# Performance work log

Measured on AMD Instinct MI355X. Metric: run time of the kernel, lower is better.

Reference implementation:

```python
import jax, jax.numpy as jnp
import numpy as np
from jax import lax

EPS = 1e-5
TEM = 10.0  # self.tem at init; tem_proportion buffer is 0 so it stays 10.0


def _conv1d(x, w, padding, dilation=1, groups=1):
    # x: [B, C, S], w: [O, I//groups, K]
    return lax.conv_general_dilated(
        x, w, window_strides=(1,), padding=[(padding, padding)],
        rhs_dilation=(dilation,), dimension_numbers=('NCH', 'OIH', 'NCH'),
        feature_group_count=groups)


def _bn(y, gamma, beta):
    # training-mode BatchNorm1d: stats over (batch, length) per channel
    m = y.mean(axis=(0, 2), keepdims=True)
    v = y.var(axis=(0, 2), keepdims=True)
    return (y - m) * lax.rsqrt(v + EPS) * gamma[None, :, None] + beta[None, :, None]


def _nor_conv(x, w, g, b, k):
    return _bn(_conv1d(jax.nn.relu(x), w, padding=k // 2), g, b)


def _dil_conv(x, wd, wp, g, b, k):
    C = x.shape[1]
    y = _conv1d(jax.nn.relu(x), wd, padding=k - 1, dilation=2, groups=C)
    y = _conv1d(y, wp, padding=0)
    return _bn(y, g, b)


def _avg_pool3(x):
    s = lax.reduce_window(x, 0.0, lax.add, (1, 1, 3), (1, 1, 1),
                          [(0, 0), (0, 0), (1, 1)])
    return s / 3.0  # count_include_pad=True


def _max_pool3(x):
    return lax.reduce_window(x, -jnp.inf, lax.max, (1, 1, 3), (1, 1, 1),
                             [(0, 0), (0, 0), (1, 1)])


def _forward(x, u, arch_parameters,
             w_nor3, g_nor3, b_nor3, w_nor5, g_nor5, b_nor5,
             w_nor7, g_nor7, b_nor7,
             wd_dil3, wp_dil3, g_dil3, b_dil3,
             wd_dil5, wp_dil5, g_dil5, b_dil5,
             wd_dil7, wp_dil7, g_dil7, b_dil7):
    # ---- Gumbel straight-through gate (get_gumbel_prob) ----
    uc = jnp.clip(u, 1e-9, 1.0 - 1e-9)
    gumbels = -jnp.log(-jnp.log(uc))  # -log(Exp(1) sample)
    logits = (jax.nn.log_softmax(arch_parameters, axis=1) + gumbels) / TEM
    probs = jax.nn.softmax(logits, axis=1)          # [1, 10]
    index = jnp.argmax(probs, axis=-1)              # [1]
    one_h = jax.nn.one_hot(index, probs.shape[-1], dtype=probs.dtype)
    hardwts = one_h - lax.stop_gradient(probs) + probs  # straight-through

    # ---- forward_gdas: single edge (max_nodes=2) ----
    xc = jnp.transpose(x, (0, 2, 1))  # [B, H, S]: hidden=channels, seq=length
    branches = [
        lambda t: jnp.zeros_like(t),                         # none
        _avg_pool3,                                          # avg_pool_3
        _max_pool3,                                          # max_pool_3
        lambda t: _nor_conv(t, w_nor3, g_nor3, b_nor3, 3),   # nor_conv_3
        lambda t: _nor_conv(t, w_nor5, g_nor5, b_nor5, 5),   # nor_conv_5
        lambda t: _nor_conv(t, w_nor7, g_nor7, b_nor7, 7),   # nor_conv_7
        lambda t: _dil_conv(t, wd_dil3, wp_dil3, g_dil3, b_dil3, 3),
        lambda t: _dil_conv(t, wd_dil5, wp_dil5, g_dil5, b_dil5, 5),
        lambda t: _dil_conv(t, wd_dil7, wp_dil7, g_dil7, b_dil7, 7),
        lambda t: t,                                         # skip_connect
    ]
    idx = index[0]
    w = hardwts[0]                                  # [10]
    sel = lax.switch(idx, branches, xc)             # only argmax op is run
    w_sel = jnp.take(w, idx)
    # GDAS: w[argmax]*op(x) + sum of remaining scalar weights (broadcast add)
    out = w_sel * sel + (jnp.sum(w) - w_sel)
    out = jnp.transpose(out, (0, 2, 1))             # back to [B, S, H]
    return out + x                                  # residual


def setup_inputs() -> dict:
    key = jax.random.key(0)
    ks = jax.random.split(key, 16)
    B, S, H = 8, 512, 768
    d = {
        'x': jax.random.normal(ks[0], (B, S, H), jnp.float32),
        'u': jax.random.uniform(ks[1], (1, 10), jnp.float32),
        'arch_parameters': 0.001 * jax.random.normal(ks[2], (1, 10), jnp.float32),
    }
    i = 3
    for k in (3, 5, 7):
        d[f'w_nor{k}'] = 0.02 * jax.random.normal(ks[i], (H, H, k), jnp.float32); i += 1
        d[f'g_nor{k}'] = jnp.ones((H,), jnp.float32)
        d[f'b_nor{k}'] = jnp.zeros((H,), jnp.float32)
    for k in (3, 5, 7):
        d[f'wd_dil{k}'] = 0.1 * jax.random.normal(ks[i], (H, 1, k), jnp.float32); i += 1
        d[f'wp_dil{k}'] = 0.02 * jax.random.normal(ks[i], (H, H, 1), jnp.float32); i += 1
        d[f'g_dil{k}'] = jnp.ones((H,), jnp.float32)
        d[f'b_dil{k}'] = jnp.zeros((H,), jnp.float32)
    return d


def reference(x, u, arch_parameters,
              w_nor3, g_nor3, b_nor3, w_nor5, g_nor5, b_nor5,
              w_nor7, g_nor7, b_nor7,
              wd_dil3, wp_dil3, g_dil3, b_dil3,
              wd_dil5, wp_dil5, g_dil5, b_dil5,
              wd_dil7, wp_dil7, g_dil7, b_dil7):
    return _forward(x, u, arch_parameters,
                    w_nor3, g_nor3, b_nor3, w_nor5, g_nor5, b_nor5,
                    w_nor7, g_nor7, b_nor7,
                    wd_dil3, wp_dil3, g_dil3, b_dil3,
                    wd_dil5, wp_dil5, g_dil5, b_dil5,
                    wd_dil7, wp_dil7, g_dil7, b_dil7)
```

## Files before the change

### kernel.cpp

```cpp
#include <hip/hip_runtime.h>
#include <math.h>

#define BB 8
#define SS 512
#define HH 768
#define NTOT (BB*SS*HH)
#define EPSBN 1e-5f
#define SPAD 4
#define SROWS (SS + 2*SPAD)

typedef __attribute__((ext_vector_type(8))) short short8v;
typedef __attribute__((ext_vector_type(4))) float float4v;

struct Params {
  const float *x, *u, *ap;
  const float *w_nor3, *g_nor3, *b_nor3;
  const float *w_nor5, *g_nor5, *b_nor5;
  const float *w_nor7, *g_nor7, *b_nor7;
  const float *wd3, *wp3, *gd3, *bd3;
  const float *wd5, *wp5, *gd5, *bd5;
  const float *wd7, *wp7, *gd7, *bd7;
  float *out;
  float *hdr;
  float *y;
  short *xb;
  short *wb;
  float *psum;
  float *psq;
};

__device__ __forceinline__ short f2bf(float f) {
  union { float f; unsigned u; } v; v.f = f;
  unsigned r = v.u + 0x7FFF + ((v.u >> 16) & 1);
  return (short)(r >> 16);
}

__device__ __forceinline__ void gate_compute(const float* __restrict__ apg,
                                             const float* __restrict__ ug,
                                             int& idx_out, float& wsel_out) {
  float ap[10], lg[10], pr[10];
  float mx = -INFINITY;
  for (int i = 0; i < 10; i++) { ap[i] = apg[i]; mx = fmaxf(mx, ap[i]); }
  float se = 0.f;
  for (int i = 0; i < 10; i++) se += expf(ap[i] - mx);
  float lse = mx + logf(se);
  float lmax = -INFINITY;
  for (int i = 0; i < 10; i++) {
    float uc = fminf(fmaxf(ug[i], 1e-9f), 1.f - 1e-9f);
    float gb = -logf(-logf(uc));
    lg[i] = ((ap[i] - lse) + gb) * 0.1f;
    lmax = fmaxf(lmax, lg[i]);
  }
  float ps = 0.f;
  for (int i = 0; i < 10; i++) { pr[i] = expf(lg[i] - lmax); ps += pr[i]; }
  int idx = 0; float best = -INFINITY;
  for (int i = 0; i < 10; i++) {
    pr[i] /= ps;
    if (pr[i] > best) { best = pr[i]; idx = i; }
  }
  idx_out = idx;
  wsel_out = (1.0f - pr[idx]) + pr[idx];
}

#define NITEMS_A (BB * SROWS * 96)
#define NITEMS   (NITEMS_A + HH * 96)
#define PREP_BLOCKS 512

template<int K>
__device__ __forceinline__ void wprep(const float* __restrict__ W, short* __restrict__ wb,
                                      int o, int i0) {
  const float* src = W + ((size_t)o * HH + i0) * K;
  float f[8 * K];
#pragma unroll
  for (int j = 0; j < 2 * K; j++) ((float4*)f)[j] = ((const float4*)src)[j];
#pragma unroll
  for (int dk = 0; dk < K; dk++) {
    short8v o8;
#pragma unroll
    for (int j = 0; j < 8; j++) o8[j] = f2bf(f[j * K + dk]);
    *(short8v*)(wb + ((size_t)dk * HH + o) * HH + i0) = o8;
  }
}

__global__ __launch_bounds__(256) void prep_kernel(Params p) {
  __shared__ int sh_idx;
  int t = threadIdx.x;
  if (t == 0) {
    int idx; float wsel;
    gate_compute(p.ap, p.u, idx, wsel);
    sh_idx = idx;
    if (blockIdx.x == 0) {
      p.hdr[0] = wsel;
      p.hdr[1] = 0.0f;
      ((int*)p.hdr)[2] = idx;
    }
  }
  __syncthreads();
  int idx = sh_idx;
  if (idx < 3 || idx > 8) return;

  if (blockIdx.x == 0) {
    for (int i = t; i < HH; i += 256) { p.psum[i] = 0.f; p.psq[i] = 0.f; }
  }

  for (int u = blockIdx.x * 256 + t; u < NITEMS; u += PREP_BLOCKS * 256) {
    if (u < NITEMS_A) {
      int c0 = (u % 96) * 8;
      int row = (u / 96) % SROWS;
      int b = u / (96 * SROWS);
      int s = row - SPAD;
      short8v o8 = (short8v){0,0,0,0,0,0,0,0};
      if (s >= 0 && s < SS) {
        float v[8];
        if (idx <= 5) {
          const float* xp = p.x + ((size_t)(b * SS + s) * HH + c0);
          float4 f0 = ((const float4*)xp)[0];
          float4 f1 = ((const float4*)xp)[1];
          v[0] = fmaxf(f0.x, 0.f); v[1] = fmaxf(f0.y, 0.f);
          v[2] = fmaxf(f0.z, 0.f); v[3] = fmaxf(f0.w, 0.f);
          v[4] = fmaxf(f1.x, 0.f); v[5] = fmaxf(f1.y, 0.f);
          v[6] = fmaxf(f1.z, 0.f); v[7] = fmaxf(f1.w, 0.f);
        } else {
          int k = 3 + 2 * (idx - 6);
          const float* wd = (idx == 6) ? p.wd3 : (idx == 7) ? p.wd5 : p.wd7;
#pragma unroll
          for (int j = 0; j < 8; j++) v[j] = 0.f;
          for (int dk = 0; dk < k; dk++) {
            int ss = s + 2 * dk - (k - 1);
            if (ss < 0 || ss >= SS) continue;
            const float* xp = p.x + ((size_t)(b * SS + ss) * HH + c0);
            float4 f0 = ((const float4*)xp)[0];
            float4 f1 = ((const float4*)xp)[1];
            float ff[8] = {f0.x, f0.y, f0.z, f0.w, f1.x, f1.y, f1.z, f1.w};
#pragma unroll
            for (int j = 0; j < 8; j++)
              v[j] += fmaxf(ff[j], 0.f) * wd[(c0 + j) * k + dk];
          }
        }
#pragma unroll
        for (int j = 0; j < 8; j++) o8[j] = f2bf(v[j]);
      }
      *(short8v*)(p.xb + (size_t)(b * SROWS + row) * HH + c0) = o8;
    } else {
      int u2 = u - NITEMS_A;
      int i0 = (u2 % 96) * 8;
      int o = u2 / 96;
      if (idx == 3)      wprep<3>(p.w_nor3, p.wb, o, i0);
      else if (idx == 4) wprep<5>(p.w_nor5, p.wb, o, i0);
      else if (idx == 5) wprep<7>(p.w_nor7, p.wb, o, i0);
      else wprep<1>((idx == 6) ? p.wp3 : (idx == 7) ? p.wp5 : p.wp7, p.wb, o, i0);
    }
  }
}

#define BM 128
#define BN 64
#define BK 64
#define AROWS 136

typedef const __attribute__((address_space(1))) unsigned int* gas_t;
typedef __attribute__((address_space(3))) unsigned int* las_t;
__device__ __forceinline__ void gload16(const void* g, void* l) {
  __builtin_amdgcn_global_load_lds((gas_t)g, (las_t)l, 16, 0, 0);
}

__global__ __launch_bounds__(256, 3) void conv_gemm_kernel(Params p) {
  int idx = ((const int*)p.hdr)[2];
  if (idx < 3 || idx > 8) return;
  bool nor = (idx <= 5);
  int taps = nor ? (3 + 2 * (idx - 3)) : 1;
  int halo = nor ? (taps >> 1) : 0;

  __shared__ __attribute__((aligned(16))) short As[AROWS * BK];
  __shared__ __attribute__((aligned(16))) short Bs[4 * BN * BK];

  int mt = blockIdx.x;
  int b = mt >> 2;
  int s0 = (mt & 3) * BM;
  int o0 = blockIdx.y * BN;

  int t = threadIdx.x;
  int lane = t & 63;
  int w = t >> 6;
  int l16 = lane & 15, quad = lane >> 4;
  int wm0 = (w >> 1) * 64;
  int wn0 = (w & 1) * 32;
  int lr = lane >> 3;
  int sw8 = ((lane & 7) ^ lr) * 8;

  const short* Ag[4];
  int abrow = b * SROWS + s0 + 8 * w + lr;
#pragma unroll
  for (int j = 0; j < 4; j++)
    Ag[j] = p.xb + (size_t)(abrow + 32 * j) * HH + sw8;
  const short* Agp = p.xb + (size_t)(b * SROWS + s0 + 128 + lr) * HH + sw8;
  const short* Bg = p.wb + (size_t)(o0 + 8 * w + lr) * HH + sw8;

  short* Asl[4];
#pragma unroll
  for (int j = 0; j < 4; j++) Asl[j] = &As[(32 * j + 8 * w) * BK];
  short* Aslp = &As[128 * BK];

  float4v acc[4][2];
#pragma unroll
  for (int mi = 0; mi < 4; mi++)
#pragma unroll
    for (int ni = 0; ni < 2; ni++) acc[mi][ni] = (float4v){0.f, 0.f, 0.f, 0.f};

  const char* Ac = (const char*)As;
  const char* Bc = (const char*)Bs;
  int bb[2][2];
#pragma unroll
  for (int ni = 0; ni < 2; ni++)
#pragma unroll
    for (int h = 0; h < 2; h++)
      bb[ni][h] = (wn0 + ni * 16 + l16) * (2 * BK) + (((h * 4 + quad) ^ (l16 & 7)) << 4);

  int np0 = taps < 4 ? taps : 4;
  int np1 = taps - np0;

  auto mm = [&](int dk, int pl) {
    int doff = dk - halo + 4;
    int rowA = wm0 + l16 + doff;
    int xr = (l16 + doff) & 7;
    int a0 = rowA * 128 + ((quad ^ xr) << 4);
    int a1 = rowA * 128 + (((4 + quad) ^ xr) << 4);
    short8v af0[4], af1[4], bf0[2], bf1[2];
#pragma unroll
    for (int mi = 0; mi < 4; mi++) {
      af0[mi] = *(const short8v*)(Ac + a0 + mi * 2048);
      af1[mi] = *(const short8v*)(Ac + a1 + mi * 2048);
    }
    int pb = pl * 8192;
#pragma unroll
    for (int ni = 0; ni < 2; ni++) {
      bf0[ni] = *(const short8v*)(Bc + pb + bb[ni][0]);
      bf1[ni] = *(const short8v*)(Bc + pb + bb[ni][1]);
    }
#pragma unroll
    for (int mi = 0; mi < 4; mi++)
#pragma unroll
      for (int ni = 0; ni < 2; ni++)
        acc[mi][ni] = __builtin_amdgcn_mfma_f32_16x16x32_bf16(af0[mi], bf0[ni], acc[mi][ni], 0, 0, 0);
#pragma unroll
    for (int mi = 0; mi < 4; mi++)
#pragma unroll
      for (int ni = 0; ni < 2; ni++)
        acc[mi][ni] = __builtin_amdgcn_mfma_f32_16x16x32_bf16(af1[mi], bf1[ni], acc[mi][ni], 0, 0, 0);
  };

  for (int k0 = 0; k0 < HH; k0 += BK) {
#pragma unroll
    for (int j = 0; j < 4; j++) gload16(Ag[j] + k0, Asl[j]);
    if (w == 0) gload16(Agp + k0, Aslp);
    for (int pl = 0; pl < np0; pl++) {
      const short* src = Bg + (size_t)pl * HH * HH + k0;
      gload16(src, &Bs[pl * 4096 + w * 512]);
      gload16(src + (size_t)32 * HH, &Bs[pl * 4096 + 2048 + w * 512]);
    }
    __syncthreads();
    for (int dk = 0; dk < np0; dk++) mm(dk, dk);
    __syncthreads();
    if (np1 > 0) {
      for (int pl = 0; pl < np1; pl++) {
        const short* src = Bg + (size_t)(4 + pl) * HH * HH + k0;
        gload16(src, &Bs[pl * 4096 + w * 512]);
        gload16(src + (size_t)32 * HH, &Bs[pl * 4096 + 2048 + w * 512]);
      }
      __syncthreads();
      for (int dk = 0; dk < np1; dk++) mm(4 + dk, dk);
      __syncthreads();
    }
  }

#pragma unroll
  for (int mi = 0; mi < 4; mi++)
#pragma unroll
    for (int ni = 0; ni < 2; ni++) {
      int col = o0 + wn0 + ni * 16 + l16;
#pragma unroll
      for (int r = 0; r < 4; r++) {
        int row = s0 + wm0 + mi * 16 + quad * 4 + r;
        p.y[((size_t)(b * SS + row)) * HH + col] = acc[mi][ni][r];
      }
    }

#pragma unroll
  for (int ni = 0; ni < 2; ni++) {
    float s = 0.f, q = 0.f;
#pragma unroll
    for (int mi = 0; mi < 4; mi++)
#pragma unroll
      for (int r = 0; r < 4; r++) { float v = acc[mi][ni][r]; s += v; q += v * v; }
    s += __shfl_xor(s, 16); s += __shfl_xor(s, 32);
    q += __shfl_xor(q, 16); q += __shfl_xor(q, 32);
    if (lane < 16) {
      int col = o0 + wn0 + ni * 16 + l16;
      atomicAdd(&p.psum[col], s);
      atomicAdd(&p.psq[col], q);
    }
  }
}

#define EPI_BLOCKS 1536
__global__ __launch_bounds__(256) void epilogue_kernel(Params p) {
  int idx = ((const int*)p.hdr)[2];
  float w_sel = p.hdr[0], w_rest = p.hdr[1];
  for (int t4 = blockIdx.x * 256 + threadIdx.x; t4 < NTOT / 4; t4 += EPI_BLOCKS * 256) {
    int base = t4 * 4;
    float4 xv = *(const float4*)(p.x + base);
    float4 sel;
    if (idx >= 3 && idx <= 8) {
      const float* g = (idx == 3) ? p.g_nor3 : (idx == 4) ? p.g_nor5 : (idx == 5) ? p.g_nor7
                     : (idx == 6) ? p.gd3 : (idx == 7) ? p.gd5 : p.gd7;
      const float* be = (idx == 3) ? p.b_nor3 : (idx == 4) ? p.b_nor5 : (idx == 5) ? p.b_nor7
                      : (idx == 6) ? p.bd3 : (idx == 7) ? p.bd5 : p.bd7;
      int c = base % HH;
      float4 yv = *(const float4*)(p.y + base);
      float4 ps = *(const float4*)(p.psum + c);
      float4 pq = *(const float4*)(p.psq + c);
      float4 gv = *(const float4*)(g + c);
      float4 bv = *(const float4*)(be + c);
      const float inv = 1.f / 4096.f;
      float m0 = ps.x * inv, m1 = ps.y * inv, m2 = ps.z * inv, m3 = ps.w * inv;
      float i0 = rsqrtf(pq.x * inv - m0 * m0 + EPSBN);
      float i1 = rsqrtf(pq.y * inv - m1 * m1 + EPSBN);
      float i2 = rsqrtf(pq.z * inv - m2 * m2 + EPSBN);
      float i3 = rsqrtf(pq.w * inv - m3 * m3 + EPSBN);
      sel.x = (yv.x - m0) * i0 * gv.x + bv.x;
      sel.y = (yv.y - m1) * i1 * gv.y + bv.y;
      sel.z = (yv.z - m2) * i2 * gv.z + bv.z;
      sel.w = (yv.w - m3) * i3 * gv.w + bv.w;
    } else if (idx == 0) {
      sel = (float4){0.f, 0.f, 0.f, 0.f};
    } else if (idx == 9) {
      sel = xv;
    } else {
      int s = (base / HH) % SS;
      float4 xm, xp;
      if (idx == 1) {
        xm = (s > 0)      ? *(const float4*)(p.x + base - HH) : (float4){0.f, 0.f, 0.f, 0.f};
        xp = (s < SS - 1) ? *(const float4*)(p.x + base + HH) : (float4){0.f, 0.f, 0.f, 0.f};
        sel.x = (xm.x + xv.x + xp.x) / 3.f;
        sel.y = (xm.y + xv.y + xp.y) / 3.f;
        sel.z = (xm.z + xv.z + xp.z) / 3.f;
        sel.w = (xm.w + xv.w + xp.w) / 3.f;
      } else {
        xm = (s > 0)      ? *(const float4*)(p.x + base - HH) : (float4){-INFINITY, -INFINITY, -INFINITY, -INFINITY};
        xp = (s < SS - 1) ? *(const float4*)(p.x + base + HH) : (float4){-INFINITY, -INFINITY, -INFINITY, -INFINITY};
        sel.x = fmaxf(fmaxf(xm.x, xv.x), xp.x);
        sel.y = fmaxf(fmaxf(xm.y, xv.y), xp.y);
        sel.z = fmaxf(fmaxf(xm.z, xv.z), xp.z);
        sel.w = fmaxf(fmaxf(xm.w, xv.w), xp.w);
      }
    }
    float4 ov;
    ov.x = w_sel * sel.x + w_rest + xv.x;
    ov.y = w_sel * sel.y + w_rest + xv.y;
    ov.z = w_sel * sel.z + w_rest + xv.z;
    ov.w = w_sel * sel.w + w_rest + xv.w;
    *(float4*)(p.out + base) = ov;
  }
}

extern "C" void kernel_launch(void* const* d_in, const int* in_sizes, int n_in,
                              void* d_out, int out_size, void* d_ws, size_t ws_size,
                              hipStream_t stream) {
  Params p;
  p.x = (const float*)d_in[0];
  p.u = (const float*)d_in[1];
  p.ap = (const float*)d_in[2];
  p.w_nor3 = (const float*)d_in[3];  p.g_nor3 = (const float*)d_in[4];  p.b_nor3 = (const float*)d_in[5];
  p.w_nor5 = (const float*)d_in[6];  p.g_nor5 = (const float*)d_in[7];  p.b_nor5 = (const float*)d_in[8];
  p.w_nor7 = (const float*)d_in[9];  p.g_nor7 = (const float*)d_in[10]; p.b_nor7 = (const float*)d_in[11];
  p.wd3 = (const float*)d_in[12]; p.wp3 = (const float*)d_in[13]; p.gd3 = (const float*)d_in[14]; p.bd3 = (const float*)d_in[15];
  p.wd5 = (const float*)d_in[16]; p.wp5 = (const float*)d_in[17]; p.gd5 = (const float*)d_in[18]; p.bd5 = (const float*)d_in[19];
  p.wd7 = (const float*)d_in[20]; p.wp7 = (const float*)d_in[21]; p.gd7 = (const float*)d_in[22]; p.bd7 = (const float*)d_in[23];
  p.out = (float*)d_out;

  char* ws = (char*)d_ws;
  size_t off = 0;
  p.hdr = (float*)(ws + off); off += 256;
  p.y   = (float*)(ws + off); off += (size_t)NTOT * 4;
  p.xb  = (short*)(ws + off); off += (size_t)BB * SROWS * HH * 2;
  p.wb  = (short*)(ws + off); off += (size_t)7 * HH * HH * 2;
  p.psum = (float*)(ws + off); off += HH * 4;
  p.psq  = (float*)(ws + off); off += HH * 4;

  hipLaunchKernelGGL(prep_kernel, dim3(PREP_BLOCKS), dim3(256), 0, stream, p);
  hipLaunchKernelGGL(conv_gemm_kernel, dim3(SS * BB / BM, HH / BN), dim3(256), 0, stream, p);
  hipLaunchKernelGGL(epilogue_kernel, dim3(EPI_BLOCKS), dim3(256), 0, stream, p);
}
```

Baseline: 134.7 us.

## Fuse prep, GEMM and epilogue into one cooperative kernel with grid syncs

Merges the three launches into a single cooperative kernel. Each block computes the gate itself, and grid-wide barriers separate the prep, conv-GEMM and epilogue phases. When the gate selects a non-conv branch, the kernel goes straight to the epilogue and skips the extra phases. This removes launch gaps and the header round-trip, but the grid is capped at 512 blocks, so the GEMM uses only 384 of them and grid.sync adds cost. If the cooperative launch fails, the code falls back to the original three-kernel path.

Result: slower. 176.7 us (+31.1%).

```diff
diff --git a/kernel.cpp b/kernel.cpp
--- a/kernel.cpp
+++ b/kernel.cpp
@@ -1,5 +1,8 @@
 #include <hip/hip_runtime.h>
+#include <hip/hip_cooperative_groups.h>
 #include <math.h>
+
+namespace cg = cooperative_groups;
 
 #define BB 8
 #define SS 512
@@ -65,6 +68,8 @@
 #define NITEMS_A (BB * SROWS * 96)
 #define NITEMS   (NITEMS_A + HH * 96)
 #define PREP_BLOCKS 512
+#define EPI_BLOCKS 1536
+#define FGRID 512
 
 template<int K>
 __device__ __forceinline__ void wprep(const float* __restrict__ W, short* __restrict__ wb,
@@ -82,28 +87,8 @@
   }
 }
 
-__global__ __launch_bounds__(256) void prep_kernel(Params p) {
-  __shared__ int sh_idx;
-  int t = threadIdx.x;
-  if (t == 0) {
-    int idx; float wsel;
-    gate_compute(p.ap, p.u, idx, wsel);
-    sh_idx = idx;
-    if (blockIdx.x == 0) {
-      p.hdr[0] = wsel;
-      p.hdr[1] = 0.0f;
-      ((int*)p.hdr)[2] = idx;
-    }
-  }
-  __syncthreads();
-  int idx = sh_idx;
-  if (idx < 3 || idx > 8) return;
-
-  if (blockIdx.x == 0) {
-    for (int i = t; i < HH; i += 256) { p.psum[i] = 0.f; p.psq[i] = 0.f; }
-  }
-
-  for (int u = blockIdx.x * 256 + t; u < NITEMS; u += PREP_BLOCKS * 256) {
+__device__ __forceinline__ void do_prep(const Params& p, int idx, int gtid, int stride) {
+  for (int u = gtid; u < NITEMS; u += stride) {
     if (u < NITEMS_A) {
       int c0 = (u % 96) * 8;
       int row = (u / 96) % SROWS;
@@ -164,20 +149,14 @@
   __builtin_amdgcn_global_load_lds((gas_t)g, (las_t)l, 16, 0, 0);
 }
 
-__global__ __launch_bounds__(256, 3) void conv_gemm_kernel(Params p) {
-  int idx = ((const int*)p.hdr)[2];
-  if (idx < 3 || idx > 8) return;
+__device__ __forceinline__ void do_gemm_tile(const Params& p, int idx, int mt, int o0,
+                                             short* As, short* Bs) {
   bool nor = (idx <= 5);
   int taps = nor ? (3 + 2 * (idx - 3)) : 1;
   int halo = nor ? (taps >> 1) : 0;
 
-  __shared__ __attribute__((aligned(16))) short As[AROWS * BK];
-  __shared__ __attribute__((aligned(16))) short Bs[4 * BN * BK];
-
-  int mt = blockIdx.x;
   int b = mt >> 2;
   int s0 = (mt & 3) * BM;
-  int o0 = blockIdx.y * BN;
 
   int t = threadIdx.x;
   int lane = t & 63;
@@ -302,11 +281,9 @@
   }
 }
 
-#define EPI_BLOCKS 1536
-__global__ __launch_bounds__(256) void epilogue_kernel(Params p) {
-  int idx = ((const int*)p.hdr)[2];
-  float w_sel = p.hdr[0], w_rest = p.hdr[1];
-  for (int t4 = blockIdx.x * 256 + threadIdx.x; t4 < NTOT / 4; t4 += EPI_BLOCKS * 256) {
+__device__ __forceinline__ void do_epilogue(const Params& p, int idx, float w_sel,
+                                            float w_rest, int gtid, int stride) {
+  for (int t4 = gtid; t4 < NTOT / 4; t4 += stride) {
     int base = t4 * 4;
     float4 xv = *(const float4*)(p.x + base);
     float4 sel;
@@ -363,6 +340,82 @@
   }
 }
 
+__global__ __launch_bounds__(256, 3) void fused_kernel(Params p) {
+  __shared__ __attribute__((aligned(16))) short As[AROWS * BK];
+  __shared__ __attribute__((aligned(16))) short Bs[4 * BN * BK];
+
+  int idx; float w_sel;
+  gate_compute(p.ap, p.u, idx, w_sel);
+  const float w_rest = 0.0f;
+
+  int gtid = blockIdx.x * 256 + threadIdx.x;
+  int stride = gridDim.x * 256;
+
+  if (idx < 3 || idx > 8) {
+    do_epilogue(p, idx, w_sel, w_rest, gtid, stride);
+    return;
+  }
+
+  cg::grid_group grid = cg::this_grid();
+
+  if (blockIdx.x == 0) {
+    for (int i = threadIdx.x; i < HH; i += 256) { p.psum[i] = 0.f; p.psq[i] = 0.f; }
+  }
+  do_prep(p, idx, gtid, stride);
+
+  __threadfence();
+  grid.sync();
+  __threadfence();
+
+  if (blockIdx.x < 384) {
+    int mt = blockIdx.x & 31;
+    int o0 = (blockIdx.x >> 5) * BN;
+    do_gemm_tile(p, idx, mt, o0, As, Bs);
+  }
+
+  __threadfence();
+  grid.sync();
+  __threadfence();
+
+  do_epilogue(p, idx, w_sel, w_rest, gtid, stride);
+}
+
+__global__ __launch_bounds__(256) void prep_kernel(Params p) {
+  __shared__ int sh_idx;
+  int t = threadIdx.x;
+  if (t == 0) {
+    int idx; float wsel;
+    gate_compute(p.ap, p.u, idx, wsel);
+    sh_idx = idx;
+    if (blockIdx.x == 0) {
+      p.hdr[0] = wsel;
+      p.hdr[1] = 0.0f;
+      ((int*)p.hdr)[2] = idx;
+    }
+  }
+  __syncthreads();
+  int idx = sh_idx;
+  if (idx < 3 || idx > 8) return;
+  if (blockIdx.x == 0) {
+    for (int i = t; i < HH; i += 256) { p.psum[i] = 0.f; p.psq[i] = 0.f; }
+  }
+  do_prep(p, idx, blockIdx.x * 256 + t, PREP_BLOCKS * 256);
+}
+
+__global__ __launch_bounds__(256, 3) void conv_gemm_kernel(Params p) {
+  int idx = ((const int*)p.hdr)[2];
+  if (idx < 3 || idx > 8) return;
+  __shared__ __attribute__((aligned(16))) short As[AROWS * BK];
+  __shared__ __attribute__((aligned(16))) short Bs[4 * BN * BK];
+  do_gemm_tile(p, idx, blockIdx.x, blockIdx.y * BN, As, Bs);
+}
+
+__global__ __launch_bounds__(256) void epilogue_kernel(Params p) {
+  int idx = ((const int*)p.hdr)[2];
+  float w_sel = p.hdr[0], w_rest = p.hdr[1];
+  do_epilogue(p, idx, w_sel, w_rest, blockIdx.x * 256 + threadIdx.x, EPI_BLOCKS * 256);
+}
+
 extern "C" void kernel_launch(void* const* d_in, const int* in_sizes, int n_in,
                               void* d_out, int out_size, void* d_ws, size_t ws_size,
                               hipStream_t stream) {
@@ -387,7 +440,12 @@
   p.psum = (float*)(ws + off); off += HH * 4;
   p.psq  = (float*)(ws + off); off += HH * 4;
 
-  hipLaunchKernelGGL(prep_kernel, dim3(PREP_BLOCKS), dim3(256), 0, stream, p);
-  hipLaunchKernelGGL(conv_gemm_kernel, dim3(SS * BB / BM, HH / BN), dim3(256), 0, stream, p);
-  hipLaunchKernelGGL(epilogue_kernel, dim3(EPI_BLOCKS), dim3(256), 0, stream, p);
-}
+  void* args[] = { (void*)&p };
+  hipError_t e = hipLaunchCooperativeKernel((const void*)fused_kernel,
+                                            dim3(FGRID), dim3(256), args, 0, stream);
+  if (e != hipSuccess) {
+    hipLaunchKernelGGL(prep_kernel, dim3(PREP_BLOCKS), dim3(256), 0, stream, p);
+    hipLaunchKernelGGL(conv_gemm_kernel, dim3(SS * BB / BM, HH / BN), dim3(256), 0, stream, p);
+    hipLaunchKernelGGL(epilogue_kernel, dim3(EPI_BLOCKS), dim3(256), 0, stream, p);
+  }
+}
```
